# Kernel optimization log

Measured on AMD Instinct MI355X. Metric: run time of the kernel, lower is better.

The kernel has to match this reference:

```python
import jax, jax.numpy as jnp
import numpy as np


def setup_inputs() -> dict:
    key = jax.random.key(0)
    ks = jax.random.split(key, 9)
    B, Lq, Lk, D = 8, 2048, 2048, 768
    s = 1.0 / np.sqrt(D)
    return {
        "queries": jax.random.normal(ks[0], (B, Lq, D), dtype=jnp.float32),
        "values": jax.random.normal(ks[1], (B, Lk, D), dtype=jnp.float32),
        "mask": jax.random.randint(ks[2], (B, Lq, Lk), 0, 2) > 0,
        "Wq": jax.random.normal(ks[3], (D, D), dtype=jnp.float32) * s,
        "bq": jax.random.normal(ks[4], (D,), dtype=jnp.float32) * s,
        "Wk": jax.random.normal(ks[5], (D, D), dtype=jnp.float32) * s,
        "bk": jax.random.normal(ks[6], (D,), dtype=jnp.float32) * s,
        "Wv": jax.random.normal(ks[7], (D, D), dtype=jnp.float32) * s,
        "bv": jax.random.normal(ks[8], (D,), dtype=jnp.float32) * s,
    }


def reference(queries, values, mask, Wq, bq, Wk, bk, Wv, bv):
    NEG = jnp.asarray(-1e9, queries.dtype)
    # torch Linear: x @ W.T + b
    q = jnp.einsum("bld,ed->ble", queries, Wq) + bq
    v = jnp.einsum("bld,ed->ble", values, Wv) + bv
    # NOTE (faithful to source): keys are the key-projection of the
    # already value-projected tensor.
    k = jnp.einsum("bld,ed->ble", v, Wk) + bk
    score = jnp.einsum("bqd,bkd->bqk", q, k)  # [B, Lq, Lk]
    score = jnp.where(mask, score, NEG)
    attn = jax.nn.sigmoid(score)  # sigmoid attention, no normalization
    context = jnp.einsum("bqk,bkd->bqd", attn, v)
    return context
```

## Files before the change

kernel.cpp:

```cpp
#include <hip/hip_runtime.h>
#include <hip/hip_bf16.h>

typedef __bf16 bf16_t;
typedef __bf16 bf16x8 __attribute__((ext_vector_type(8)));
typedef __bf16 bf16x4 __attribute__((ext_vector_type(4)));
typedef float  f32x4  __attribute__((ext_vector_type(4)));

#define LDS_DST(p) ((__attribute__((address_space(3))) void*)(p))
#define GLB_SRC(p) ((const __attribute__((address_space(1))) void*)(p))

#define SBAR()   asm volatile("s_barrier" ::: "memory")
#define WVM6()   asm volatile("s_waitcnt vmcnt(6)" ::: "memory")
#define WVM0()   asm volatile("s_waitcnt vmcnt(0)" ::: "memory")
#define SP1()    __builtin_amdgcn_s_setprio(1)
#define SP0()    __builtin_amdgcn_s_setprio(0)

__global__ void __launch_bounds__(256)
f32_to_bf16_kernel(const float* __restrict__ in, bf16_t* __restrict__ out, int n4) {
  int i = blockIdx.x * 256 + threadIdx.x;
  if (i < n4) {
    const float4 v = reinterpret_cast<const float4*>(in)[i];
    bf16x4 o;
    o[0] = (bf16_t)v.x; o[1] = (bf16_t)v.y; o[2] = (bf16_t)v.z; o[3] = (bf16_t)v.w;
    reinterpret_cast<bf16x4*>(out)[i] = o;
  }
}

__global__ void __launch_bounds__(256)
mask_pack_kernel(const int* __restrict__ mask, unsigned long long* __restrict__ bits) {
  const long wid = (((long)blockIdx.x * 256 + threadIdx.x) >> 6);
  const int lane = threadIdx.x & 63;
  const long base = wid * 512;
  unsigned long long b[8];
#pragma unroll
  for (int i = 0; i < 8; ++i) {
    const int m = mask[base + i * 64 + lane];
    b[i] = __ballot(m != 0);
  }
  if (lane == 0) {
    unsigned long long* o = bits + wid * 8;
#pragma unroll
    for (int i = 0; i < 8; ++i) o[i] = b[i];
  }
}

__global__ void __launch_bounds__(256)
transpose_bf16_kernel(const bf16_t* __restrict__ in, bf16_t* __restrict__ out,
                      int R, int C) {
  __shared__ bf16_t tile[64][72];
  const long base = (long)blockIdx.z * R * C;
  const bf16_t* ib = in + base;
  bf16_t* ob = out + base;
  const int r0 = blockIdx.x * 64, c0 = blockIdx.y * 64;
  const int tid = threadIdx.x;
  const int rr = tid >> 3, cg = tid & 7;
#pragma unroll
  for (int p = 0; p < 2; ++p) {
    int row = p * 32 + rr;
    bf16x8 v = *reinterpret_cast<const bf16x8*>(ib + (long)(r0 + row) * C + c0 + cg * 8);
    *reinterpret_cast<bf16x8*>(&tile[row][cg * 8]) = v;
  }
  __syncthreads();
#pragma unroll
  for (int p = 0; p < 2; ++p) {
    int c = p * 32 + rr;
    bf16x8 v;
#pragma unroll
    for (int i = 0; i < 8; ++i) v[i] = tile[cg * 8 + i][c];
    *reinterpret_cast<bf16x8*>(ob + (long)(c0 + c) * R + r0 + cg * 8) = v;
  }
}


__device__ __forceinline__ void stage_A(char* smem, const bf16_t* G, int ldK,
                                        int grow0, int slot, int mh, int kt, int tid) {
  const int wave = tid >> 6, l = tid & 63;
  const int lr = l >> 3;
  const int cgs = ((l & 7) ^ lr) * 8;
#pragma unroll
  for (int j = 0; j < 2; ++j) {
    const int rowbase = j * 128 + mh * 64 + wave * 8;
    __builtin_amdgcn_global_load_lds(
        GLB_SRC(G + (long)(grow0 + rowbase + lr) * ldK + kt + cgs),
        LDS_DST(smem + slot * 65536 + rowbase * 128), 16, 0, 0);
  }
}

__device__ __forceinline__ void stage_B(char* smem, const bf16_t* G, int ldK,
                                        int grow0, int slot, int nh, int kt, int tid) {
  const int wave = tid >> 6, l = tid & 63;
  const int lr = l >> 3;
  const int cgs = ((l & 7) ^ lr) * 8;
#pragma unroll
  for (int j = 0; j < 2; ++j) {
    const int c = wave + j * 8;
    const int rowbase = (c >> 2) * 64 + nh * 32 + (c & 3) * 8;
    __builtin_amdgcn_global_load_lds(
        GLB_SRC(G + (long)(grow0 + rowbase + lr) * ldK + kt + cgs),
        LDS_DST(smem + slot * 65536 + 32768 + rowbase * 128), 16, 0, 0);
  }
}

__device__ __forceinline__ void read_A(const char* smem, int off, bf16x8 (&af)[8], int xk0) {
#pragma unroll
  for (int mf = 0; mf < 4; ++mf)
#pragma unroll
    for (int kk = 0; kk < 2; ++kk)
      af[mf * 2 + kk] = *reinterpret_cast<const bf16x8*>(
          smem + off + mf * 2048 + (kk ? (xk0 ^ 64) : xk0));
}

__device__ __forceinline__ void read_B(const char* smem, int off, bf16x8 (&bf_)[4], int xk0) {
#pragma unroll
  for (int nf = 0; nf < 2; ++nf)
#pragma unroll
    for (int kk = 0; kk < 2; ++kk)
      bf_[nf * 2 + kk] = *reinterpret_cast<const bf16x8*>(
          smem + off + nf * 2048 + (kk ? (xk0 ^ 64) : xk0));
}

template <int MH, int NH>
__device__ __forceinline__ void mfma_q(const bf16x8 (&af)[8], const bf16x8 (&bf_)[4],
                                       f32x4 (&acc)[8][4]) {
#pragma unroll
  for (int mf = 0; mf < 4; ++mf)
#pragma unroll
    for (int nf = 0; nf < 2; ++nf)
#pragma unroll
      for (int kk = 0; kk < 2; ++kk)
        acc[MH * 4 + mf][NH * 2 + nf] = __builtin_amdgcn_mfma_f32_16x16x32_bf16(
            af[mf * 2 + kk], bf_[nf * 2 + kk], acc[MH * 4 + mf][NH * 2 + nf], 0, 0, 0);
}

template <int MODE>
__global__ void __launch_bounds__(512, 2)
gemm8p_kernel(const bf16_t* __restrict__ A, const bf16_t* __restrict__ B,
              const float* __restrict__ bias, const unsigned* __restrict__ maskbits,
              void* __restrict__ Cout, int M, int N, int K,
              long sA, long sB, long sC, long sMask) {
  __shared__ __align__(1024) char smem[131072];
  const int bz = blockIdx.z;
  const bf16_t* Ab = A + bz * sA;
  const bf16_t* Bb = B + bz * sB;
  const int bm = blockIdx.x * 256, bn = blockIdx.y * 256;
  const int tid = threadIdx.x;
  const int wave = tid >> 6, lane = tid & 63;
  const int wr = wave >> 2, wc = wave & 3;
  const int l15 = lane & 15, lg = lane >> 4;
  const int xk0 = (lg * 16) ^ ((lane & 7) << 4);
  const int NT = K >> 6;

  const int aoff = wr * 16384 + l15 * 128;
  const int boff = 32768 + wc * 8192 + l15 * 128;

  f32x4 acc[8][4] = {};
  bf16x8 af[8], bf_[4];

  stage_A(smem, Ab, K, bm, 0, 0, 0, tid);
  stage_B(smem, Bb, K, bn, 0, 0, 0, tid);
  stage_B(smem, Bb, K, bn, 0, 1, 0, tid);
  stage_A(smem, Ab, K, bm, 0, 1, 0, tid);
  stage_A(smem, Ab, K, bm, 1, 0, 64, tid);
  stage_B(smem, Bb, K, bn, 1, 1, 64, tid);
  stage_A(smem, Ab, K, bm, 1, 1, 64, tid);
  WVM6();
  SBAR();

  int tp = 0;
  for (; tp + 3 < NT; tp += 2) {
    const int kb = (tp + 1) << 6, kc = (tp + 2) << 6, kd = (tp + 3) << 6;
    read_A(smem, aoff + 0, af, xk0);
    read_B(smem, boff + 0, bf_, xk0);
    stage_B(smem, Bb, K, bn, 1, 0, kb, tid);
    SP1(); mfma_q<0, 0>(af, bf_, acc); SP0(); SBAR();
    read_B(smem, boff + 4096, bf_, xk0);
    stage_A(smem, Ab, K, bm, 0, 0, kc, tid);
    SP1(); mfma_q<0, 1>(af, bf_, acc); SP0(); SBAR();
    read_A(smem, aoff + 8192, af, xk0);
    stage_B(smem, Bb, K, bn, 0, 1, kc, tid);
    SP1(); mfma_q<1, 1>(af, bf_, acc); SP0(); SBAR();
    read_B(smem, boff + 0, bf_, xk0);
    stage_A(smem, Ab, K, bm, 0, 1, kc, tid);
    SP1(); mfma_q<1, 0>(af, bf_, acc); SP0(); WVM6(); SBAR();
    read_A(smem, aoff + 65536, af, xk0);
    read_B(smem, boff + 65536, bf_, xk0);
    stage_B(smem, Bb, K, bn, 0, 0, kc, tid);
    SP1(); mfma_q<0, 0>(af, bf_, acc); SP0(); SBAR();
    read_B(smem, boff + 65536 + 4096, bf_, xk0);
    stage_A(smem, Ab, K, bm, 1, 0, kd, tid);
    SP1(); mfma_q<0, 1>(af, bf_, acc); SP0(); SBAR();
    read_A(smem, aoff + 65536 + 8192, af, xk0);
    stage_B(smem, Bb, K, bn, 1, 1, kd, tid);
    SP1(); mfma_q<1, 1>(af, bf_, acc); SP0(); SBAR();
    read_B(smem, boff + 65536, bf_, xk0);
    stage_A(smem, Ab, K, bm, 1, 1, kd, tid);
    SP1(); mfma_q<1, 0>(af, bf_, acc); SP0(); WVM6(); SBAR();
  }

  {
    const int kb = (NT - 1) << 6;
    read_A(smem, aoff + 0, af, xk0);
    read_B(smem, boff + 0, bf_, xk0);
    stage_B(smem, Bb, K, bn, 1, 0, kb, tid);
    SP1(); mfma_q<0, 0>(af, bf_, acc); SP0(); SBAR();
    read_B(smem, boff + 4096, bf_, xk0);
    SP1(); mfma_q<0, 1>(af, bf_, acc); SP0(); SBAR();
    read_A(smem, aoff + 8192, af, xk0);
    SP1(); mfma_q<1, 1>(af, bf_, acc); SP0(); SBAR();
    read_B(smem, boff + 0, bf_, xk0);
    SP1(); mfma_q<1, 0>(af, bf_, acc); SP0(); WVM0(); SBAR();
    read_A(smem, aoff + 65536, af, xk0);
    read_B(smem, boff + 65536, bf_, xk0);
    SP1(); mfma_q<0, 0>(af, bf_, acc); SP0(); SBAR();
    read_B(smem, boff + 65536 + 4096, bf_, xk0);
    SP1(); mfma_q<0, 1>(af, bf_, acc); SP0(); SBAR();
    read_A(smem, aoff + 65536 + 8192, af, xk0);
    SP1(); mfma_q<1, 1>(af, bf_, acc); SP0(); SBAR();
    read_B(smem, boff + 65536, bf_, xk0);
    SP1(); mfma_q<1, 0>(af, bf_, acc); SP0();
  }

  float* eb = (float*)smem;
  const int lrow = tid >> 3, t7 = tid & 7;
#pragma unroll
  for (int rd = 0; rd < 4; ++rd) {
    __syncthreads();
#pragma unroll
    for (int fi = 0; fi < 2; ++fi)
#pragma unroll
      for (int nf = 0; nf < 4; ++nf)
#pragma unroll
        for (int r = 0; r < 4; ++r) {
          const int lr2 = wr * 32 + fi * 16 + lg * 4 + r;
          eb[lr2 * 256 + wc * 64 + nf * 16 + l15] = acc[rd * 2 + fi][nf][r];
        }
    __syncthreads();
    const int growt = rd * 32 + lrow + ((lrow >> 5) * 96);
    const long rowbase = (long)(bm + growt) * N + bn;
    if constexpr (MODE == 1) {
      const unsigned* mw =
          maskbits + bz * sMask + (long)(bm + growt) * (N >> 5) + (bn >> 5);
      const uint4 w0 = *reinterpret_cast<const uint4*>(mw);
      const uint4 w1 = *reinterpret_cast<const uint4*>(mw + 4);
      const unsigned wq[8] = {w0.x, w0.y, w0.z, w0.w, w1.x, w1.y, w1.z, w1.w};
#pragma unroll
      for (int q = 0; q < 8; ++q) {
        const int c4 = (q * 8 + t7) * 4;
        const f32x4 v = *reinterpret_cast<const f32x4*>(&eb[lrow * 256 + c4]);
        const unsigned nib = (wq[q] >> (t7 * 4)) & 0xFu;
        bf16x4 o;
        o[0] = (bf16_t)((nib & 1u) ? 1.f / (1.f + __expf(-v[0])) : 0.f);
        o[1] = (bf16_t)((nib & 2u) ? 1.f / (1.f + __expf(-v[1])) : 0.f);
        o[2] = (bf16_t)((nib & 4u) ? 1.f / (1.f + __expf(-v[2])) : 0.f);
        o[3] = (bf16_t)((nib & 8u) ? 1.f / (1.f + __expf(-v[3])) : 0.f);
        *reinterpret_cast<bf16x4*>((bf16_t*)Cout + bz * sC + rowbase + c4) = o;
      }
    } else {
#pragma unroll
      for (int q = 0; q < 8; ++q) {
        const int c4 = (q * 8 + t7) * 4;
        const f32x4 v = *reinterpret_cast<const f32x4*>(&eb[lrow * 256 + c4]);
        if constexpr (MODE == 0) {
          const f32x4 b4 = *reinterpret_cast<const f32x4*>(bias + bn + c4);
          bf16x4 o;
          o[0] = (bf16_t)(v[0] + b4[0]); o[1] = (bf16_t)(v[1] + b4[1]);
          o[2] = (bf16_t)(v[2] + b4[2]); o[3] = (bf16_t)(v[3] + b4[3]);
          *reinterpret_cast<bf16x4*>((bf16_t*)Cout + bz * sC + rowbase + c4) = o;
        } else {
          *reinterpret_cast<f32x4*>((float*)Cout + bz * sC + rowbase + c4) = v;
        }
      }
    }
  }
}

extern "C" void kernel_launch(void* const* d_in, const int* in_sizes, int n_in,
                              void* d_out, int out_size, void* d_ws, size_t ws_size,
                              hipStream_t stream) {
  const float* queries = (const float*)d_in[0];
  const float* values  = (const float*)d_in[1];
  const int*   mask    = (const int*)d_in[2];
  const float* Wq = (const float*)d_in[3];
  const float* bq = (const float*)d_in[4];
  const float* Wk = (const float*)d_in[5];
  const float* bk = (const float*)d_in[6];
  const float* Wv = (const float*)d_in[7];
  const float* bv = (const float*)d_in[8];

  char* ws = (char*)d_ws;
  bf16_t* qb  = (bf16_t*)(ws + 0);
  bf16_t* vb  = (bf16_t*)(ws + 25165824);
  bf16_t* wqb = (bf16_t*)(ws + 50331648);
  bf16_t* wkb = (bf16_t*)(ws + 51511296);
  bf16_t* wvb = (bf16_t*)(ws + 52690944);
  bf16_t* qp  = (bf16_t*)(ws + 53870592);
  bf16_t* vp  = (bf16_t*)(ws + 79036416);
  bf16_t* kp  = (bf16_t*)(ws + 104202240);
  bf16_t* vpT = (bf16_t*)(ws + 129368064);
  bf16_t* P   = (bf16_t*)(ws + 154533888);
  unsigned long long* mbits = (unsigned long long*)(ws + 221642752);

  mask_pack_kernel<<<16384, 256, 0, stream>>>(mask, mbits);

  f32_to_bf16_kernel<<<12288, 256, 0, stream>>>(queries, qb, 3145728);
  f32_to_bf16_kernel<<<12288, 256, 0, stream>>>(values, vb, 3145728);
  f32_to_bf16_kernel<<<576, 256, 0, stream>>>(Wq, wqb, 147456);
  f32_to_bf16_kernel<<<576, 256, 0, stream>>>(Wk, wkb, 147456);
  f32_to_bf16_kernel<<<576, 256, 0, stream>>>(Wv, wvb, 147456);

  const dim3 blk2(512);

  gemm8p_kernel<0><<<dim3(64, 3, 1), blk2, 0, stream>>>(
      qb, wqb, bq, nullptr, qp, 16384, 768, 768, 0, 0, 0, 0);
  gemm8p_kernel<0><<<dim3(64, 3, 1), blk2, 0, stream>>>(
      vb, wvb, bv, nullptr, vp, 16384, 768, 768, 0, 0, 0, 0);
  gemm8p_kernel<0><<<dim3(64, 3, 1), blk2, 0, stream>>>(
      vp, wkb, bk, nullptr, kp, 16384, 768, 768, 0, 0, 0, 0);

  transpose_bf16_kernel<<<dim3(32, 12, 8), 256, 0, stream>>>(vp, vpT, 2048, 768);

  gemm8p_kernel<1><<<dim3(8, 8, 8), blk2, 0, stream>>>(
      qp, kp, nullptr, (const unsigned*)mbits, P, 2048, 2048, 768,
      (long)2048 * 768, (long)2048 * 768, (long)2048 * 2048, (long)2048 * 64);

  gemm8p_kernel<2><<<dim3(8, 3, 8), blk2, 0, stream>>>(
      P, vpT, nullptr, nullptr, d_out, 2048, 768, 2048,
      (long)2048 * 2048, (long)768 * 2048, (long)2048 * 768, 0);
}
```

Before: 303.2 us.

## Restructure GEMM main loop into single-tile ping-pong pipeline and vectorize mask packing

```diff
diff --git a/kernel.cpp b/kernel.cpp
--- a/kernel.cpp
+++ b/kernel.cpp
@@ -10,7 +10,9 @@
 #define GLB_SRC(p) ((const __attribute__((address_space(1))) void*)(p))
 
 #define SBAR()   asm volatile("s_barrier" ::: "memory")
+#define WVM8()   asm volatile("s_waitcnt vmcnt(8)" ::: "memory")
 #define WVM6()   asm volatile("s_waitcnt vmcnt(6)" ::: "memory")
+#define WVM2()   asm volatile("s_waitcnt vmcnt(2)" ::: "memory")
 #define WVM0()   asm volatile("s_waitcnt vmcnt(0)" ::: "memory")
 #define SP1()    __builtin_amdgcn_s_setprio(1)
 #define SP0()    __builtin_amdgcn_s_setprio(0)
@@ -27,21 +29,19 @@
 }
 
 __global__ void __launch_bounds__(256)
-mask_pack_kernel(const int* __restrict__ mask, unsigned long long* __restrict__ bits) {
-  const long wid = (((long)blockIdx.x * 256 + threadIdx.x) >> 6);
-  const int lane = threadIdx.x & 63;
-  const long base = wid * 512;
-  unsigned long long b[8];
-#pragma unroll
-  for (int i = 0; i < 8; ++i) {
-    const int m = mask[base + i * 64 + lane];
-    b[i] = __ballot(m != 0);
-  }
-  if (lane == 0) {
-    unsigned long long* o = bits + wid * 8;
-#pragma unroll
-    for (int i = 0; i < 8; ++i) o[i] = b[i];
-  }
+mask_pack_kernel(const int* __restrict__ mask, unsigned* __restrict__ bits) {
+  const long i = (long)blockIdx.x * 256 + threadIdx.x;
+  const int4* m4 = reinterpret_cast<const int4*>(mask + i * 32);
+  unsigned w = 0;
+#pragma unroll
+  for (int j = 0; j < 8; ++j) {
+    const int4 v = m4[j];
+    w |= (v.x != 0 ? 1u : 0u) << (j * 4);
+    w |= (v.y != 0 ? 2u : 0u) << (j * 4);
+    w |= (v.z != 0 ? 4u : 0u) << (j * 4);
+    w |= (v.w != 0 ? 8u : 0u) << (j * 4);
+  }
+  bits[i] = w;
 }
 
 __global__ void __launch_bounds__(256)
@@ -72,35 +72,6 @@
 }
 
 
-__device__ __forceinline__ void stage_A(char* smem, const bf16_t* G, int ldK,
-                                        int grow0, int slot, int mh, int kt, int tid) {
-  const int wave = tid >> 6, l = tid & 63;
-  const int lr = l >> 3;
-  const int cgs = ((l & 7) ^ lr) * 8;
-#pragma unroll
-  for (int j = 0; j < 2; ++j) {
-    const int rowbase = j * 128 + mh * 64 + wave * 8;
-    __builtin_amdgcn_global_load_lds(
-        GLB_SRC(G + (long)(grow0 + rowbase + lr) * ldK + kt + cgs),
-        LDS_DST(smem + slot * 65536 + rowbase * 128), 16, 0, 0);
-  }
-}
-
-__device__ __forceinline__ void stage_B(char* smem, const bf16_t* G, int ldK,
-                                        int grow0, int slot, int nh, int kt, int tid) {
-  const int wave = tid >> 6, l = tid & 63;
-  const int lr = l >> 3;
-  const int cgs = ((l & 7) ^ lr) * 8;
-#pragma unroll
-  for (int j = 0; j < 2; ++j) {
-    const int c = wave + j * 8;
-    const int rowbase = (c >> 2) * 64 + nh * 32 + (c & 3) * 8;
-    __builtin_amdgcn_global_load_lds(
-        GLB_SRC(G + (long)(grow0 + rowbase + lr) * ldK + kt + cgs),
-        LDS_DST(smem + slot * 65536 + 32768 + rowbase * 128), 16, 0, 0);
-  }
-}
-
 __device__ __forceinline__ void read_A(const char* smem, int off, bf16x8 (&af)[8], int xk0) {
 #pragma unroll
   for (int mf = 0; mf < 4; ++mf)
@@ -131,6 +102,23 @@
         acc[MH * 4 + mf][NH * 2 + nf] = __builtin_amdgcn_mfma_f32_16x16x32_bf16(
             af[mf * 2 + kk], bf_[nf * 2 + kk], acc[MH * 4 + mf][NH * 2 + nf], 0, 0, 0);
 }
+
+#define STAGE_A(slot, mh, kt) do {                                            \
+  _Pragma("unroll") for (int j_ = 0; j_ < 2; ++j_)                            \
+    __builtin_amdgcn_global_load_lds(                                         \
+        GLB_SRC(pA + (long)(j_ * 128 + (mh) * 64) * K + (kt)),                \
+        LDS_DST(smem + (slot) * 65536 + (arow0 + j_ * 128 + (mh) * 64) * 128),\
+        16, 0, 0);                                                            \
+} while (0)
+
+#define STAGE_B(slot, nh, kt) do {                                            \
+  _Pragma("unroll") for (int j_ = 0; j_ < 2; ++j_)                            \
+    __builtin_amdgcn_global_load_lds(                                         \
+        GLB_SRC(pB + (long)(j_ * 128 + (nh) * 32) * K + (kt)),                \
+        LDS_DST(smem + (slot) * 65536 + 32768 +                               \
+                (brow0 + j_ * 128 + (nh) * 32) * 128),                        \
+        16, 0, 0);                                                            \
+} while (0)
 
 template <int MODE>
 __global__ void __launch_bounds__(512, 2)
@@ -150,74 +138,65 @@
   const int xk0 = (lg * 16) ^ ((lane & 7) << 4);
   const int NT = K >> 6;
 
+  const int lr = lane >> 3;
+  const int cgs = ((lane & 7) ^ lr) * 8;
+  const int arow0 = wave * 8;
+  const int brow0 = (wave >> 2) * 64 + (wave & 3) * 8;
+  const bf16_t* pA = Ab + (long)(bm + arow0 + lr) * K + cgs;
+  const bf16_t* pB = Bb + (long)(bn + brow0 + lr) * K + cgs;
+
   const int aoff = wr * 16384 + l15 * 128;
   const int boff = 32768 + wc * 8192 + l15 * 128;
 
   f32x4 acc[8][4] = {};
-  bf16x8 af[8], bf_[4];
-
-  stage_A(smem, Ab, K, bm, 0, 0, 0, tid);
-  stage_B(smem, Bb, K, bn, 0, 0, 0, tid);
-  stage_B(smem, Bb, K, bn, 0, 1, 0, tid);
-  stage_A(smem, Ab, K, bm, 0, 1, 0, tid);
-  stage_A(smem, Ab, K, bm, 1, 0, 64, tid);
-  stage_B(smem, Bb, K, bn, 1, 1, 64, tid);
-  stage_A(smem, Ab, K, bm, 1, 1, 64, tid);
-  WVM6();
+  bf16x8 afX[8], afY[8], bfB[4], bf0[4];
+
+  STAGE_A(0, 0, 0); STAGE_B(0, 0, 0); STAGE_B(0, 1, 0); STAGE_A(0, 1, 0);
+  STAGE_A(1, 0, 64); STAGE_B(1, 0, 64); STAGE_B(1, 1, 64); STAGE_A(1, 1, 64);
+  WVM8();
   SBAR();
-
-  int tp = 0;
-  for (; tp + 3 < NT; tp += 2) {
-    const int kb = (tp + 1) << 6, kc = (tp + 2) << 6, kd = (tp + 3) << 6;
-    read_A(smem, aoff + 0, af, xk0);
-    read_B(smem, boff + 0, bf_, xk0);
-    stage_B(smem, Bb, K, bn, 1, 0, kb, tid);
-    SP1(); mfma_q<0, 0>(af, bf_, acc); SP0(); SBAR();
-    read_B(smem, boff + 4096, bf_, xk0);
-    stage_A(smem, Ab, K, bm, 0, 0, kc, tid);
-    SP1(); mfma_q<0, 1>(af, bf_, acc); SP0(); SBAR();
-    read_A(smem, aoff + 8192, af, xk0);
-    stage_B(smem, Bb, K, bn, 0, 1, kc, tid);
-    SP1(); mfma_q<1, 1>(af, bf_, acc); SP0(); SBAR();
-    read_B(smem, boff + 0, bf_, xk0);
-    stage_A(smem, Ab, K, bm, 0, 1, kc, tid);
-    SP1(); mfma_q<1, 0>(af, bf_, acc); SP0(); WVM6(); SBAR();
-    read_A(smem, aoff + 65536, af, xk0);
-    read_B(smem, boff + 65536, bf_, xk0);
-    stage_B(smem, Bb, K, bn, 0, 0, kc, tid);
-    SP1(); mfma_q<0, 0>(af, bf_, acc); SP0(); SBAR();
-    read_B(smem, boff + 65536 + 4096, bf_, xk0);
-    stage_A(smem, Ab, K, bm, 1, 0, kd, tid);
-    SP1(); mfma_q<0, 1>(af, bf_, acc); SP0(); SBAR();
-    read_A(smem, aoff + 65536 + 8192, af, xk0);
-    stage_B(smem, Bb, K, bn, 1, 1, kd, tid);
-    SP1(); mfma_q<1, 1>(af, bf_, acc); SP0(); SBAR();
-    read_B(smem, boff + 65536, bf_, xk0);
-    stage_A(smem, Ab, K, bm, 1, 1, kd, tid);
-    SP1(); mfma_q<1, 0>(af, bf_, acc); SP0(); WVM6(); SBAR();
+  read_A(smem, aoff + 0, afX, xk0);
+  read_B(smem, boff + 0, bf0, xk0);
+
+  int slot = 0;
+  for (int t = 0; t + 2 < NT; ++t) {
+    const int so = slot * 65536, sn = (slot ^ 1) * 65536;
+    const int k2 = (t + 2) << 6;
+    read_B(smem, so + boff + 4096, bfB, xk0);
+    STAGE_A(slot, 0, k2);
+    SP1(); mfma_q<0, 0>(afX, bf0, acc); SP0();
+    read_A(smem, so + aoff + 8192, afY, xk0);
+    STAGE_B(slot, 0, k2);
+    SP1(); mfma_q<0, 1>(afX, bfB, acc); SP0();
+    WVM6(); SBAR();
+    read_A(smem, sn + aoff + 0, afX, xk0);
+    STAGE_B(slot, 1, k2);
+    SP1(); mfma_q<1, 1>(afY, bfB, acc); SP0();
+    SP1(); mfma_q<1, 0>(afY, bf0, acc); SP0();
+    read_B(smem, sn + boff + 0, bf0, xk0);
+    STAGE_A(slot, 1, k2);
+    WVM6(); SBAR();
+    slot ^= 1;
   }
 
   {
-    const int kb = (NT - 1) << 6;
-    read_A(smem, aoff + 0, af, xk0);
-    read_B(smem, boff + 0, bf_, xk0);
-    stage_B(smem, Bb, K, bn, 1, 0, kb, tid);
-    SP1(); mfma_q<0, 0>(af, bf_, acc); SP0(); SBAR();
-    read_B(smem, boff + 4096, bf_, xk0);
-    SP1(); mfma_q<0, 1>(af, bf_, acc); SP0(); SBAR();
-    read_A(smem, aoff + 8192, af, xk0);
-    SP1(); mfma_q<1, 1>(af, bf_, acc); SP0(); SBAR();
-    read_B(smem, boff + 0, bf_, xk0);
-    SP1(); mfma_q<1, 0>(af, bf_, acc); SP0(); WVM0(); SBAR();
-    read_A(smem, aoff + 65536, af, xk0);
-    read_B(smem, boff + 65536, bf_, xk0);
-    SP1(); mfma_q<0, 0>(af, bf_, acc); SP0(); SBAR();
-    read_B(smem, boff + 65536 + 4096, bf_, xk0);
-    SP1(); mfma_q<0, 1>(af, bf_, acc); SP0(); SBAR();
-    read_A(smem, aoff + 65536 + 8192, af, xk0);
-    SP1(); mfma_q<1, 1>(af, bf_, acc); SP0(); SBAR();
-    read_B(smem, boff + 65536, bf_, xk0);
-    SP1(); mfma_q<1, 0>(af, bf_, acc); SP0();
+    const int so = slot * 65536, sn = (slot ^ 1) * 65536;
+    read_B(smem, so + boff + 4096, bfB, xk0);
+    SP1(); mfma_q<0, 0>(afX, bf0, acc); SP0();
+    read_A(smem, so + aoff + 8192, afY, xk0);
+    SP1(); mfma_q<0, 1>(afX, bfB, acc); SP0();
+    WVM2(); SBAR();
+    read_A(smem, sn + aoff + 0, afX, xk0);
+    SP1(); mfma_q<1, 1>(afY, bfB, acc); SP0();
+    SP1(); mfma_q<1, 0>(afY, bf0, acc); SP0();
+    read_B(smem, sn + boff + 0, bf0, xk0);
+    WVM0(); SBAR();
+    read_B(smem, sn + boff + 4096, bfB, xk0);
+    SP1(); mfma_q<0, 0>(afX, bf0, acc); SP0();
+    read_A(smem, sn + aoff + 8192, afY, xk0);
+    SP1(); mfma_q<0, 1>(afX, bfB, acc); SP0();
+    SP1(); mfma_q<1, 1>(afY, bfB, acc); SP0();
+    SP1(); mfma_q<1, 0>(afY, bf0, acc); SP0();
   }
 
   float* eb = (float*)smem;
@@ -298,9 +277,9 @@
   bf16_t* kp  = (bf16_t*)(ws + 104202240);
   bf16_t* vpT = (bf16_t*)(ws + 129368064);
   bf16_t* P   = (bf16_t*)(ws + 154533888);
-  unsigned long long* mbits = (unsigned long long*)(ws + 221642752);
-
-  mask_pack_kernel<<<16384, 256, 0, stream>>>(mask, mbits);
+  unsigned* mbits = (unsigned*)(ws + 221642752);
+
+  mask_pack_kernel<<<4096, 256, 0, stream>>>(mask, mbits);
 
   f32_to_bf16_kernel<<<12288, 256, 0, stream>>>(queries, qb, 3145728);
   f32_to_bf16_kernel<<<12288, 256, 0, stream>>>(values, vb, 3145728);
@@ -320,7 +299,7 @@
   transpose_bf16_kernel<<<dim3(32, 12, 8), 256, 0, stream>>>(vp, vpT, 2048, 768);
 
   gemm8p_kernel<1><<<dim3(8, 8, 8), blk2, 0, stream>>>(
-      qp, kp, nullptr, (const unsigned*)mbits, P, 2048, 2048, 768,
+      qp, kp, nullptr, mbits, P, 2048, 2048, 768,
       (long)2048 * 768, (long)2048 * 768, (long)2048 * 2048, (long)2048 * 64);
 
   gemm8p_kernel<2><<<dim3(8, 3, 8), blk2, 0, stream>>>(
```

After: 516.2 us. +70.3%, slower.
